# Optimization experiments

Measured on AMD Instinct MI355X. Metric: run time of the kernel, lower is better.

Reference implementation:

```python
import jax, jax.numpy as jnp
import numpy as np

N_HEADS = 8
NEG_INF = -1e9


def setup_inputs() -> dict:
    key = jax.random.key(0)
    ks = jax.random.split(key, 9)
    B, S, D = 4, 2048, 512
    scale = 1.0 / np.sqrt(D)
    x = jax.random.normal(ks[0], (B, S, D), dtype=jnp.float32)
    mask = jnp.tril(jnp.ones((S, S), dtype=bool))[None, None, :, :]  # causal [1,1,S,S]
    W_Q_w = jax.random.normal(ks[1], (D, D), dtype=jnp.float32) * scale
    W_Q_b = jax.random.normal(ks[2], (D,), dtype=jnp.float32) * 0.02
    W_K_w = jax.random.normal(ks[3], (D, D), dtype=jnp.float32) * scale
    W_K_b = jax.random.normal(ks[4], (D,), dtype=jnp.float32) * 0.02
    W_V_w = jax.random.normal(ks[5], (D, D), dtype=jnp.float32) * scale
    W_V_b = jax.random.normal(ks[6], (D,), dtype=jnp.float32) * 0.02
    W_O_w = jax.random.normal(ks[7], (D, D), dtype=jnp.float32) * scale
    W_O_b = jax.random.normal(ks[8], (D,), dtype=jnp.float32) * 0.02
    return {"x": x, "mask": mask,
            "W_Q_w": W_Q_w, "W_Q_b": W_Q_b, "W_K_w": W_K_w, "W_K_b": W_K_b,
            "W_V_w": W_V_w, "W_V_b": W_V_b, "W_O_w": W_O_w, "W_O_b": W_O_b}


def reference(x, mask, W_Q_w, W_Q_b, W_K_w, W_K_b, W_V_w, W_V_b, W_O_w, W_O_b):
    B, S, D = x.shape
    H = N_HEADS
    Dh = D // H
    # projections (torch Linear: x @ W.T + b), split heads -> [B,H,S,Dh]
    def split_heads(t):
        return t.reshape(B, S, H, Dh).transpose(0, 2, 1, 3)
    Q = split_heads(x @ W_Q_w.T + W_Q_b)
    K = split_heads(x @ W_K_w.T + W_K_b)
    V = split_heads(x @ W_V_w.T + W_V_b)
    # scaled dot-product attention with explicit [B,H,S,S] scores
    scores = jnp.einsum("bhqd,bhkd->bhqk", Q, K) / jnp.sqrt(jnp.float32(Dh))
    scores = jnp.where(mask, scores, jnp.float32(NEG_INF))
    att = jax.nn.softmax(scores, axis=-1)
    out = jnp.einsum("bhqk,bhkd->bhqd", att, V)
    out = out.transpose(0, 2, 1, 3).reshape(B, S, D)
    return out @ W_O_w.T + W_O_b
```

## Files before the change

kernel.cpp:

```cpp
#include <hip/hip_runtime.h>
#include <hip/hip_bf16.h>

#define BATCH 4
#define SEQ   2048
#define DIM   512
#define NH    8
#define DH    64
#define NTOK  (BATCH*SEQ)

typedef __bf16 bf16x8 __attribute__((ext_vector_type(8)));
typedef float  f32x4  __attribute__((ext_vector_type(4)));

#define MFMA16(a,b,c) __builtin_amdgcn_mfma_f32_16x16x32_bf16((a),(b),(c),0,0,0)

__global__ __launch_bounds__(256) void cvt_f32_bf16(const float* __restrict__ src,
                                                    __bf16* __restrict__ dst, int n8) {
  int i = blockIdx.x * blockDim.x + threadIdx.x;
  if (i >= n8) return;
  const float4* s = (const float4*)src;
  float4 a = s[2*i], b = s[2*i+1];
  bf16x8 o;
  o[0] = (__bf16)a.x; o[1] = (__bf16)a.y; o[2] = (__bf16)a.z; o[3] = (__bf16)a.w;
  o[4] = (__bf16)b.x; o[5] = (__bf16)b.y; o[6] = (__bf16)b.z; o[7] = (__bf16)b.w;
  *(bf16x8*)&dst[8*i] = o;
}

__global__ __launch_bounds__(256) void cvt_weights(
    const float* __restrict__ s0, const float* __restrict__ s1,
    const float* __restrict__ s2, const float* __restrict__ s3,
    __bf16* __restrict__ o0, __bf16* __restrict__ o1,
    __bf16* __restrict__ o2, __bf16* __restrict__ o3) {
  int i = blockIdx.x * blockDim.x + threadIdx.x;
  const int which = i >> 15, off = i & 32767;
  const float* src = (which == 0) ? s0 : (which == 1) ? s1 : (which == 2) ? s2 : s3;
  __bf16* dst      = (which == 0) ? o0 : (which == 1) ? o1 : (which == 2) ? o2 : o3;
  const float4* s = (const float4*)src;
  float4 a = s[2*off], b = s[2*off+1];
  bf16x8 o;
  o[0] = (__bf16)a.x; o[1] = (__bf16)a.y; o[2] = (__bf16)a.z; o[3] = (__bf16)a.w;
  o[4] = (__bf16)b.x; o[5] = (__bf16)b.y; o[6] = (__bf16)b.z; o[7] = (__bf16)b.w;
  *(bf16x8*)&dst[8*off] = o;
}

__global__ __launch_bounds__(256) void gemm_qkv(
    const __bf16* __restrict__ xb,
    const __bf16* __restrict__ wq, const __bf16* __restrict__ wk,
    const __bf16* __restrict__ wv,
    const float* __restrict__ bq, const float* __restrict__ bk,
    const float* __restrict__ bv,
    __bf16* __restrict__ Qb, __bf16* __restrict__ Kb, __bf16* __restrict__ Vt)
{
  const int z = blockIdx.z;
  const __bf16* W    = (z == 0) ? wq : (z == 1) ? wk : wv;
  const float*  bias = (z == 0) ? bq : (z == 1) ? bk : bv;

  __shared__ __bf16 As[128*72];
  __shared__ __bf16 Bs[128*72];

  const int tid  = threadIdx.x;
  const int m0   = blockIdx.x * 128, n0 = blockIdx.y * 128;
  const int w    = tid >> 6, lane = tid & 63, quad = lane >> 4, l16 = lane & 15;
  const int wm   = (w >> 1) * 64, wn = (w & 1) * 64;

  f32x4 acc[4][4] = {};

  for (int k0 = 0; k0 < DIM; k0 += 64) {
#pragma unroll
    for (int i = 0; i < 4; ++i) {
      int c   = tid + i * 256;
      int row = c >> 3;
      int kc  = (c & 7) << 3;
      *(bf16x8*)&As[row*72 + kc] = *(const bf16x8*)&xb[(size_t)(m0+row)*DIM + k0 + kc];
      *(bf16x8*)&Bs[row*72 + kc] = *(const bf16x8*)&W [(size_t)(n0+row)*DIM + k0 + kc];
    }
    __syncthreads();
#pragma unroll
    for (int kk = 0; kk < 2; ++kk) {
      const int ko = kk*32 + quad*8;
      bf16x8 af[4], bfr[4];
#pragma unroll
      for (int f = 0; f < 4; ++f) {
        af[f]  = *(const bf16x8*)&As[(wm + f*16 + l16)*72 + ko];
        bfr[f] = *(const bf16x8*)&Bs[(wn + f*16 + l16)*72 + ko];
      }
#pragma unroll
      for (int fm = 0; fm < 4; ++fm)
#pragma unroll
        for (int fn = 0; fn < 4; ++fn)
          acc[fm][fn] = MFMA16(af[fm], bfr[fn], acc[fm][fn]);
    }
    __syncthreads();
  }

#pragma unroll
  for (int fm = 0; fm < 4; ++fm) {
#pragma unroll
    for (int fn = 0; fn < 4; ++fn) {
      const int col  = n0 + wn + fn*16 + l16;
      const float bc = bias[col];
      const int h = col >> 6, dh = col & 63;
#pragma unroll
      for (int r = 0; r < 4; ++r) {
        const int row = m0 + wm + fm*16 + quad*4 + r;
        const int b = row >> 11, s = row & 2047;
        const float v = acc[fm][fn][r] + bc;
        if (z == 2) {
          Vt[((size_t)(b*NH + h)*DH + dh)*SEQ + s] = (__bf16)v;
        } else {
          __bf16* O = (z == 0) ? Qb : Kb;
          O[((size_t)(b*NH + h)*SEQ + s)*DH + dh] = (__bf16)v;
        }
      }
    }
  }
}

__global__ __launch_bounds__(256) void gemm_out(
    const __bf16* __restrict__ attnb, const __bf16* __restrict__ wo,
    const float* __restrict__ bo, float* __restrict__ out)
{
  __shared__ __bf16 As[128*72];
  __shared__ __bf16 Bs[128*72];

  const int tid = threadIdx.x;
  const int m0  = blockIdx.x * 128, n0 = blockIdx.y * 128;
  const int w   = tid >> 6, lane = tid & 63, quad = lane >> 4, l16 = lane & 15;
  const int wm  = (w >> 1) * 64, wn = (w & 1) * 64;

  f32x4 acc[4][4] = {};

  for (int k0 = 0; k0 < DIM; k0 += 64) {
#pragma unroll
    for (int i = 0; i < 4; ++i) {
      int c   = tid + i * 256;
      int row = c >> 3;
      int kc  = (c & 7) << 3;
      *(bf16x8*)&As[row*72 + kc] = *(const bf16x8*)&attnb[(size_t)(m0+row)*DIM + k0 + kc];
      *(bf16x8*)&Bs[row*72 + kc] = *(const bf16x8*)&wo   [(size_t)(n0+row)*DIM + k0 + kc];
    }
    __syncthreads();
#pragma unroll
    for (int kk = 0; kk < 2; ++kk) {
      const int ko = kk*32 + quad*8;
      bf16x8 af[4], bfr[4];
#pragma unroll
      for (int f = 0; f < 4; ++f) {
        af[f]  = *(const bf16x8*)&As[(wm + f*16 + l16)*72 + ko];
        bfr[f] = *(const bf16x8*)&Bs[(wn + f*16 + l16)*72 + ko];
      }
#pragma unroll
      for (int fm = 0; fm < 4; ++fm)
#pragma unroll
        for (int fn = 0; fn < 4; ++fn)
          acc[fm][fn] = MFMA16(af[fm], bfr[fn], acc[fm][fn]);
    }
    __syncthreads();
  }

#pragma unroll
  for (int fm = 0; fm < 4; ++fm) {
#pragma unroll
    for (int fn = 0; fn < 4; ++fn) {
      const int col  = n0 + wn + fn*16 + l16;
      const float bc = bo[col];
#pragma unroll
      for (int r = 0; r < 4; ++r) {
        const int row = m0 + wm + fm*16 + quad*4 + r;
        out[(size_t)row*DIM + col] = acc[fm][fn][r] + bc;
      }
    }
  }
}

__global__ __launch_bounds__(64) void flash_attn(
    const __bf16* __restrict__ Qb, const __bf16* __restrict__ Kb,
    const __bf16* __restrict__ Vt, __bf16* __restrict__ attnb)
{
  const int idx = blockIdx.x;
  const int bh  = idx & 31;
  const int t   = 63 - (idx >> 5);
  const int b   = bh >> 3, h = bh & 7;
  const int lane = threadIdx.x & 63, quad = lane >> 4, l16 = lane & 15;
  const int q0  = t * 32;

  const __bf16* Qp = Qb + (size_t)bh * SEQ * DH;
  const __bf16* Kp = Kb + (size_t)bh * SEQ * DH;
  const __bf16* Vp = Vt + (size_t)bh * DH * SEQ;

  __shared__ __bf16 Pw[32*72];

  bf16x8 qf[2][2];
#pragma unroll
  for (int mf = 0; mf < 2; ++mf)
#pragma unroll
    for (int kk = 0; kk < 2; ++kk) {
      bf16x8 q = *(const bf16x8*)&Qp[(size_t)(q0 + mf*16 + l16)*DH + kk*32 + quad*8];
#pragma unroll
      for (int j = 0; j < 8; ++j) q[j] = (__bf16)((float)q[j] * 0.125f);
      qf[mf][kk] = q;
    }

  f32x4 of[2][4] = {};
  float m_[2][4], l_[2][4];
#pragma unroll
  for (int mf = 0; mf < 2; ++mf)
#pragma unroll
    for (int r = 0; r < 4; ++r) { m_[mf][r] = -1e30f; l_[mf][r] = 0.f; }

  const int ktiles = (q0 >> 6) + 1;

  bf16x8 kfA[4][2], kfB[4][2];
#pragma unroll
  for (int fn = 0; fn < 4; ++fn)
#pragma unroll
    for (int kk = 0; kk < 2; ++kk)
      kfA[fn][kk] = *(const bf16x8*)&Kp[(size_t)(fn*16 + l16)*DH + kk*32 + quad*8];

#define TILE_STEP(KC, KN, KT)                                                  \
  {                                                                            \
    const int k0 = (KT) * 64;                                                  \
                   \
    bf16x8 vf[4][2];                                                           \
    _Pragma("unroll")                                                          \
    for (int nd = 0; nd < 4; ++nd)                                             \
      _Pragma("unroll")                                                        \
      for (int kq = 0; kq < 2; ++kq)                                           \
        vf[nd][kq] = *(const bf16x8*)&Vp[(size_t)(nd*16 + l16)*SEQ + k0 +      \
                                         kq*32 + quad*8];                      \
                               \
    {                                                                          \
      const int kn0 = ((KT) + 1 < ktiles) ? k0 + 64 : 0;                       \
      _Pragma("unroll")                                                        \
      for (int fn = 0; fn < 4; ++fn)                                           \
        _Pragma("unroll")                                                      \
        for (int kk = 0; kk < 2; ++kk)                                         \
          KN[fn][kk] = *(const bf16x8*)&Kp[(size_t)(kn0 + fn*16 + l16)*DH +    \
                                           kk*32 + quad*8];                    \
    }                                                                          \
                                            \
    f32x4 sf[2][4] = {};                                                       \
    _Pragma("unroll")                                                          \
    for (int mf = 0; mf < 2; ++mf)                                             \
      _Pragma("unroll")                                                        \
      for (int fn = 0; fn < 4; ++fn) {                                         \
        sf[mf][fn] = MFMA16(qf[mf][0], KC[fn][0], sf[mf][fn]);                 \
        sf[mf][fn] = MFMA16(qf[mf][1], KC[fn][1], sf[mf][fn]);                 \
      }                                                                        \
                            \
    if (k0 + 63 > q0) {                                                        \
      _Pragma("unroll")                                                        \
      for (int mf = 0; mf < 2; ++mf)                                           \
        _Pragma("unroll")                                                      \
        for (int fn = 0; fn < 4; ++fn) {                                       \
          const int col = k0 + fn*16 + l16;                                    \
          _Pragma("unroll")                                                    \
          for (int r = 0; r < 4; ++r) {                                        \
            const int row = q0 + mf*16 + quad*4 + r;                           \
            if (col > row) sf[mf][fn][r] = -1e30f;                             \
          }                                                                    \
        }                                                                      \
    }                                                                          \
                                        \
    float rmax[2][4];                                                          \
    _Pragma("unroll")                                                          \
    for (int mf = 0; mf < 2; ++mf)                                             \
      _Pragma("unroll")                                                        \
      for (int r = 0; r < 4; ++r)                                              \
        rmax[mf][r] = fmaxf(fmaxf(sf[mf][0][r], sf[mf][1][r]),                 \
                            fmaxf(sf[mf][2][r], sf[mf][3][r]));                \
    _Pragma("unroll")                                                          \
    for (int d = 1; d < 16; d <<= 1)                                           \
      _Pragma("unroll")                                                        \
      for (int mf = 0; mf < 2; ++mf)                                           \
        _Pragma("unroll")                                                      \
        for (int r = 0; r < 4; ++r)                                            \
          rmax[mf][r] = fmaxf(rmax[mf][r], __shfl_xor(rmax[mf][r], d));        \
    _Pragma("unroll")                                                          \
    for (int mf = 0; mf < 2; ++mf)                                             \
      _Pragma("unroll")                                                        \
      for (int r = 0; r < 4; ++r) {                                            \
        const float mn = fmaxf(m_[mf][r], rmax[mf][r]);                        \
        const float al = __expf(m_[mf][r] - mn);                               \
        m_[mf][r] = mn;                                                        \
        l_[mf][r] *= al;                                                       \
        _Pragma("unroll")                                                      \
        for (int nd = 0; nd < 4; ++nd) of[mf][nd][r] *= al;                    \
      }                                                                        \
    _Pragma("unroll")                                                          \
    for (int mf = 0; mf < 2; ++mf)                                             \
      _Pragma("unroll")                                                        \
      for (int fn = 0; fn < 4; ++fn)                                           \
        _Pragma("unroll")                                                      \
        for (int r = 0; r < 4; ++r)                                            \
          sf[mf][fn][r] = __expf(sf[mf][fn][r] - m_[mf][r]);                   \
    float rsum[2][4];                                                          \
    _Pragma("unroll")                                                          \
    for (int mf = 0; mf < 2; ++mf)                                             \
      _Pragma("unroll")                                                        \
      for (int r = 0; r < 4; ++r)                                              \
        rsum[mf][r] = (sf[mf][0][r] + sf[mf][1][r]) +                          \
                      (sf[mf][2][r] + sf[mf][3][r]);                           \
    _Pragma("unroll")                                                          \
    for (int d = 1; d < 16; d <<= 1)                                           \
      _Pragma("unroll")                                                        \
      for (int mf = 0; mf < 2; ++mf)                                           \
        _Pragma("unroll")                                                      \
        for (int r = 0; r < 4; ++r)                                            \
          rsum[mf][r] += __shfl_xor(rsum[mf][r], d);                           \
    _Pragma("unroll")                                                          \
    for (int mf = 0; mf < 2; ++mf)                                             \
      _Pragma("unroll")                                                        \
      for (int r = 0; r < 4; ++r) l_[mf][r] += rsum[mf][r];                    \
                                           \
    _Pragma("unroll")                                                          \
    for (int mf = 0; mf < 2; ++mf)                                             \
      _Pragma("unroll")                                                        \
      for (int fn = 0; fn < 4; ++fn)                                           \
        _Pragma("unroll")                                                      \
        for (int r = 0; r < 4; ++r)                                            \
          Pw[(mf*16 + quad*4 + r)*72 + fn*16 + l16] = (__bf16)sf[mf][fn][r];   \
    bf16x8 pa[2][2];                                                           \
    _Pragma("unroll")                                                          \
    for (int mf = 0; mf < 2; ++mf)                                             \
      _Pragma("unroll")                                                        \
      for (int kq = 0; kq < 2; ++kq)                                           \
        pa[mf][kq] = *(const bf16x8*)&Pw[(mf*16 + l16)*72 + kq*32 + quad*8];   \
                                                      \
    _Pragma("unroll")                                                          \
    for (int mf = 0; mf < 2; ++mf)                                             \
      _Pragma("unroll")                                                        \
      for (int nd = 0; nd < 4; ++nd) {                                         \
        of[mf][nd] = MFMA16(pa[mf][0], vf[nd][0], of[mf][nd]);                 \
        of[mf][nd] = MFMA16(pa[mf][1], vf[nd][1], of[mf][nd]);                 \
      }                                                                        \
  }

  for (int kt = 0; kt < ktiles; kt += 2) {
    TILE_STEP(kfA, kfB, kt);
    if (kt + 1 < ktiles) TILE_STEP(kfB, kfA, kt + 1);
  }
#undef TILE_STEP

#pragma unroll
  for (int mf = 0; mf < 2; ++mf)
#pragma unroll
    for (int r = 0; r < 4; ++r)
      l_[mf][r] = 1.0f / l_[mf][r];
#pragma unroll
  for (int mf = 0; mf < 2; ++mf)
#pragma unroll
    for (int nd = 0; nd < 4; ++nd) {
      const int dh = nd*16 + l16;
#pragma unroll
      for (int r = 0; r < 4; ++r) {
        const int q = q0 + mf*16 + quad*4 + r;
        attnb[((size_t)b*SEQ + q)*DIM + h*DH + dh] = (__bf16)(of[mf][nd][r] * l_[mf][r]);
      }
    }
}

extern "C" void kernel_launch(void* const* d_in, const int* in_sizes, int n_in,
                              void* d_out, int out_size, void* d_ws, size_t ws_size,
                              hipStream_t stream) {
  const float* x  = (const float*)d_in[0];
  const float* Wq = (const float*)d_in[2];
  const float* bq = (const float*)d_in[3];
  const float* Wk = (const float*)d_in[4];
  const float* bk = (const float*)d_in[5];
  const float* Wv = (const float*)d_in[6];
  const float* bv = (const float*)d_in[7];
  const float* Wo = (const float*)d_in[8];
  const float* bo = (const float*)d_in[9];
  float* out = (float*)d_out;

  __bf16* xb    = (__bf16*)d_ws;
  __bf16* wq    = xb + (size_t)NTOK*DIM;
  __bf16* wk    = wq + DIM*DIM;
  __bf16* wv    = wk + DIM*DIM;
  __bf16* wo    = wv + DIM*DIM;
  __bf16* Qb    = wo + DIM*DIM;
  __bf16* Kb    = Qb + (size_t)NTOK*DIM;
  __bf16* Vt    = Kb + (size_t)NTOK*DIM;
  __bf16* attnb = Vt + (size_t)NTOK*DIM;

  cvt_f32_bf16<<<(NTOK*DIM/8)/256, 256, 0, stream>>>(x, xb, NTOK*DIM/8);
  cvt_weights<<<(4*DIM*DIM/8)/256, 256, 0, stream>>>(Wq, Wk, Wv, Wo, wq, wk, wv, wo);

  gemm_qkv<<<dim3(NTOK/128, DIM/128, 3), 256, 0, stream>>>(
      xb, wq, wk, wv, bq, bk, bv, Qb, Kb, Vt);

  flash_attn<<<2048, 64, 0, stream>>>(Qb, Kb, Vt, attnb);

  gemm_out<<<dim3(NTOK/128, DIM/128), 256, 0, stream>>>(attnb, wo, bo, out);
}
```

Measured before the change: 211.3 us.

## Split attention KV loop across four waves and use async LDS loads in GEMMs

Flash attention now launches 256 threads per block. The KV tile range is split across four waves, and each wave keeps its own running max and sum; the partial outputs are merged through shared memory with a log-sum-exp rescale before a single vectorized store. The QKV and output GEMMs switch to global_load_lds direct-to-LDS copies with unpadded 64-wide rows. The QKV epilogue now stages results in an XOR-swizzled LDS tile so that Q, K and the transposed V are written with coalesced 16-byte stores. Together these aim to raise occupancy and parallelism on long causal rows and to remove scattered 2-byte global writes. The cost is an extra reduction with serialized syncs in attention, and the unpadded LDS reads in the GEMMs risk bank conflicts.

```diff
diff --git a/kernel.cpp b/kernel.cpp
--- a/kernel.cpp
+++ b/kernel.cpp
@@ -12,6 +12,12 @@
 typedef float  f32x4  __attribute__((ext_vector_type(4)));
 
 #define MFMA16(a,b,c) __builtin_amdgcn_mfma_f32_16x16x32_bf16((a),(b),(c),0,0,0)
+
+__device__ __forceinline__ void async_ld16(const __bf16* g, __bf16* l) {
+  __builtin_amdgcn_global_load_lds(
+      (const __attribute__((address_space(1))) void*)g,
+      (__attribute__((address_space(3))) void*)l, 16, 0, 0);
+}
 
 __global__ __launch_bounds__(256) void cvt_f32_bf16(const float* __restrict__ src,
                                                     __bf16* __restrict__ dst, int n8) {
@@ -54,24 +60,28 @@
   const __bf16* W    = (z == 0) ? wq : (z == 1) ? wk : wv;
   const float*  bias = (z == 0) ? bq : (z == 1) ? bk : bv;
 
-  __shared__ __bf16 As[128*72];
-  __shared__ __bf16 Bs[128*72];
+  __shared__ __bf16 S[2][128*64];
+  __bf16* As = S[0];
+  __bf16* Bs = S[1];
 
   const int tid  = threadIdx.x;
   const int m0   = blockIdx.x * 128, n0 = blockIdx.y * 128;
   const int w    = tid >> 6, lane = tid & 63, quad = lane >> 4, l16 = lane & 15;
   const int wm   = (w >> 1) * 64, wn = (w & 1) * 64;
+  const int lrow = lane >> 3;
+  const int lcol = (lane & 7) * 8;
 
   f32x4 acc[4][4] = {};
 
+  const __bf16* Ag = xb + (size_t)m0 * DIM;
+  const __bf16* Bg = W  + (size_t)n0 * DIM;
+
   for (int k0 = 0; k0 < DIM; k0 += 64) {
 #pragma unroll
     for (int i = 0; i < 4; ++i) {
-      int c   = tid + i * 256;
-      int row = c >> 3;
-      int kc  = (c & 7) << 3;
-      *(bf16x8*)&As[row*72 + kc] = *(const bf16x8*)&xb[(size_t)(m0+row)*DIM + k0 + kc];
-      *(bf16x8*)&Bs[row*72 + kc] = *(const bf16x8*)&W [(size_t)(n0+row)*DIM + k0 + kc];
+      const int rb = w*32 + i*8;
+      async_ld16(&Ag[(size_t)(rb + lrow)*DIM + k0 + lcol], &As[rb*64]);
+      async_ld16(&Bg[(size_t)(rb + lrow)*DIM + k0 + lcol], &Bs[rb*64]);
     }
     __syncthreads();
 #pragma unroll
@@ -80,8 +90,8 @@
       bf16x8 af[4], bfr[4];
 #pragma unroll
       for (int f = 0; f < 4; ++f) {
-        af[f]  = *(const bf16x8*)&As[(wm + f*16 + l16)*72 + ko];
-        bfr[f] = *(const bf16x8*)&Bs[(wn + f*16 + l16)*72 + ko];
+        af[f]  = *(const bf16x8*)&As[(wm + f*16 + l16)*64 + ko];
+        bfr[f] = *(const bf16x8*)&Bs[(wn + f*16 + l16)*64 + ko];
       }
 #pragma unroll
       for (int fm = 0; fm < 4; ++fm)
@@ -92,24 +102,59 @@
     __syncthreads();
   }
 
-#pragma unroll
-  for (int fm = 0; fm < 4; ++fm) {
-#pragma unroll
-    for (int fn = 0; fn < 4; ++fn) {
-      const int col  = n0 + wn + fn*16 + l16;
-      const float bc = bias[col];
-      const int h = col >> 6, dh = col & 63;
-#pragma unroll
-      for (int r = 0; r < 4; ++r) {
-        const int row = m0 + wm + fm*16 + quad*4 + r;
-        const int b = row >> 11, s = row & 2047;
-        const float v = acc[fm][fn][r] + bc;
-        if (z == 2) {
-          Vt[((size_t)(b*NH + h)*DH + dh)*SEQ + s] = (__bf16)v;
-        } else {
-          __bf16* O = (z == 0) ? Qb : Kb;
-          O[((size_t)(b*NH + h)*SEQ + s)*DH + dh] = (__bf16)v;
+  __bf16* Cs = &S[0][0];
+  if (z < 2) {
+#pragma unroll
+    for (int fm = 0; fm < 4; ++fm)
+#pragma unroll
+      for (int fn = 0; fn < 4; ++fn) {
+        const int col = wn + fn*16 + l16;
+        const float bc = bias[n0 + col];
+        const int chunk = col >> 3, ce = col & 7;
+#pragma unroll
+        for (int r = 0; r < 4; ++r) {
+          const int row = wm + fm*16 + quad*4 + r;
+          Cs[row*128 + ((chunk ^ (row & 7)) << 3) + ce] = (__bf16)(acc[fm][fn][r] + bc);
         }
+      }
+  } else {
+#pragma unroll
+    for (int fm = 0; fm < 4; ++fm)
+#pragma unroll
+      for (int fn = 0; fn < 4; ++fn) {
+        const int dhcol = wn + fn*16 + l16;
+        const float bc = bias[n0 + dhcol];
+        const int sbase = wm + fm*16 + quad*4;
+        const int schunk = sbase >> 3, so = sbase & 7;
+        __bf16* p = &Cs[dhcol*128 + ((schunk ^ (dhcol & 7)) << 3) + so];
+#pragma unroll
+        for (int r = 0; r < 4; ++r)
+          p[r] = (__bf16)(acc[fm][fn][r] + bc);
+      }
+  }
+  __syncthreads();
+  {
+    const int row = tid >> 1, half = tid & 1;
+    if (z < 2) {
+      __bf16* O = (z == 0) ? Qb : Kb;
+      const int s = m0 + row, bb = s >> 11, ss = s & 2047;
+#pragma unroll
+      for (int j = 0; j < 8; ++j) {
+        const int chunk = half*8 + j;
+        bf16x8 v = *(const bf16x8*)&Cs[row*128 + ((chunk ^ (row & 7)) << 3)];
+        const int colg = n0 + chunk*8;
+        const int hh = colg >> 6, dh = colg & 63;
+        *(bf16x8*)&O[((size_t)(bb*NH + hh)*SEQ + ss)*DH + dh] = v;
+      }
+    } else {
+      const int colg = n0 + row;
+      const int hh = colg >> 6, dh = colg & 63;
+      const int bb = m0 >> 11, s0s = m0 & 2047;
+#pragma unroll
+      for (int j = 0; j < 8; ++j) {
+        const int chunk = half*8 + j;
+        bf16x8 v = *(const bf16x8*)&Cs[row*128 + ((chunk ^ (row & 7)) << 3)];
+        *(bf16x8*)&Vt[((size_t)(bb*NH + hh)*DH + dh)*SEQ + s0s + chunk*8] = v;
       }
     }
   }
@@ -119,24 +164,27 @@
     const __bf16* __restrict__ attnb, const __bf16* __restrict__ wo,
     const float* __restrict__ bo, float* __restrict__ out)
 {
-  __shared__ __bf16 As[128*72];
-  __shared__ __bf16 Bs[128*72];
+  __shared__ __bf16 S[2][128*64];
+  __bf16* As = S[0];
+  __bf16* Bs = S[1];
 
   const int tid = threadIdx.x;
   const int m0  = blockIdx.x * 128, n0 = blockIdx.y * 128;
   const int w   = tid >> 6, lane = tid & 63, quad = lane >> 4, l16 = lane & 15;
   const int wm  = (w >> 1) * 64, wn = (w & 1) * 64;
+  const int lrow = lane >> 3, lcol = (lane & 7) * 8;
 
   f32x4 acc[4][4] = {};
 
+  const __bf16* Ag = attnb + (size_t)m0 * DIM;
+  const __bf16* Bg = wo    + (size_t)n0 * DIM;
+
   for (int k0 = 0; k0 < DIM; k0 += 64) {
 #pragma unroll
     for (int i = 0; i < 4; ++i) {
-      int c   = tid + i * 256;
-      int row = c >> 3;
-      int kc  = (c & 7) << 3;
-      *(bf16x8*)&As[row*72 + kc] = *(const bf16x8*)&attnb[(size_t)(m0+row)*DIM + k0 + kc];
-      *(bf16x8*)&Bs[row*72 + kc] = *(const bf16x8*)&wo   [(size_t)(n0+row)*DIM + k0 + kc];
+      const int rb = w*32 + i*8;
+      async_ld16(&Ag[(size_t)(rb + lrow)*DIM + k0 + lcol], &As[rb*64]);
+      async_ld16(&Bg[(size_t)(rb + lrow)*DIM + k0 + lcol], &Bs[rb*64]);
     }
     __syncthreads();
 #pragma unroll
@@ -145,8 +193,8 @@
       bf16x8 af[4], bfr[4];
 #pragma unroll
       for (int f = 0; f < 4; ++f) {
-        af[f]  = *(const bf16x8*)&As[(wm + f*16 + l16)*72 + ko];
-        bfr[f] = *(const bf16x8*)&Bs[(wn + f*16 + l16)*72 + ko];
+        af[f]  = *(const bf16x8*)&As[(wm + f*16 + l16)*64 + ko];
+        bfr[f] = *(const bf16x8*)&Bs[(wn + f*16 + l16)*64 + ko];
       }
 #pragma unroll
       for (int fm = 0; fm < 4; ++fm)
@@ -172,22 +220,26 @@
   }
 }
 
-__global__ __launch_bounds__(64) void flash_attn(
+__global__ __launch_bounds__(256) void flash_attn(
     const __bf16* __restrict__ Qb, const __bf16* __restrict__ Kb,
     const __bf16* __restrict__ Vt, __bf16* __restrict__ attnb)
 {
   const int idx = blockIdx.x;
   const int bh  = idx & 31;
-  const int t   = 63 - (idx >> 5);
+  const int qt  = 63 - (idx >> 5);
   const int b   = bh >> 3, h = bh & 7;
-  const int lane = threadIdx.x & 63, quad = lane >> 4, l16 = lane & 15;
-  const int q0  = t * 32;
+  const int tid = threadIdx.x;
+  const int w   = tid >> 6, lane = tid & 63, quad = lane >> 4, l16 = lane & 15;
+  const int q0  = qt * 32;
 
   const __bf16* Qp = Qb + (size_t)bh * SEQ * DH;
   const __bf16* Kp = Kb + (size_t)bh * SEQ * DH;
   const __bf16* Vp = Vt + (size_t)bh * DH * SEQ;
 
-  __shared__ __bf16 Pw[32*72];
+  __shared__ __bf16 Plds[4][32*72];
+  __shared__ float  OaccL[32*68];
+  __shared__ float  mL[4][32], lL[4][32];
+  __bf16* Pw = Plds[w];
 
   bf16x8 qf[2][2];
 #pragma unroll
@@ -207,19 +259,22 @@
 #pragma unroll
     for (int r = 0; r < 4; ++r) { m_[mf][r] = -1e30f; l_[mf][r] = 0.f; }
 
-  const int ktiles = (q0 >> 6) + 1;
-
-  bf16x8 kfA[4][2], kfB[4][2];
-#pragma unroll
-  for (int fn = 0; fn < 4; ++fn)
-#pragma unroll
-    for (int kk = 0; kk < 2; ++kk)
-      kfA[fn][kk] = *(const bf16x8*)&Kp[(size_t)(fn*16 + l16)*DH + kk*32 + quad*8];
+  const int nt  = (q0 >> 6) + 1;
+  const int c   = (nt + 3) >> 2;
+  const int ktb = w * c;
+  const int kte = (ktb + c < nt) ? (ktb + c) : nt;
+
+  if (ktb < kte) {
+    bf16x8 kfA[4][2], kfB[4][2];
+#pragma unroll
+    for (int fn = 0; fn < 4; ++fn)
+#pragma unroll
+      for (int kk = 0; kk < 2; ++kk)
+        kfA[fn][kk] = *(const bf16x8*)&Kp[(size_t)(ktb*64 + fn*16 + l16)*DH + kk*32 + quad*8];
 
 #define TILE_STEP(KC, KN, KT)                                                  \
   {                                                                            \
     const int k0 = (KT) * 64;                                                  \
-                   \
     bf16x8 vf[4][2];                                                           \
     _Pragma("unroll")                                                          \
     for (int nd = 0; nd < 4; ++nd)                                             \
@@ -227,9 +282,8 @@
       for (int kq = 0; kq < 2; ++kq)                                           \
         vf[nd][kq] = *(const bf16x8*)&Vp[(size_t)(nd*16 + l16)*SEQ + k0 +      \
                                          kq*32 + quad*8];                      \
-                               \
     {                                                                          \
-      const int kn0 = ((KT) + 1 < ktiles) ? k0 + 64 : 0;                       \
+      const int kn0 = ((KT) + 1 < kte) ? k0 + 64 : k0;                         \
       _Pragma("unroll")                                                        \
       for (int fn = 0; fn < 4; ++fn)                                           \
         _Pragma("unroll")                                                      \
@@ -237,7 +291,6 @@
           KN[fn][kk] = *(const bf16x8*)&Kp[(size_t)(kn0 + fn*16 + l16)*DH +    \
                                            kk*32 + quad*8];                    \
     }                                                                          \
-                                            \
     f32x4 sf[2][4] = {};                                                       \
     _Pragma("unroll")                                                          \
     for (int mf = 0; mf < 2; ++mf)                                             \
@@ -246,7 +299,6 @@
         sf[mf][fn] = MFMA16(qf[mf][0], KC[fn][0], sf[mf][fn]);                 \
         sf[mf][fn] = MFMA16(qf[mf][1], KC[fn][1], sf[mf][fn]);                 \
       }                                                                        \
-                            \
     if (k0 + 63 > q0) {                                                        \
       _Pragma("unroll")                                                        \
       for (int mf = 0; mf < 2; ++mf)                                           \
@@ -260,7 +312,6 @@
           }                                                                    \
         }                                                                      \
     }                                                                          \
-                                        \
     float rmax[2][4];                                                          \
     _Pragma("unroll")                                                          \
     for (int mf = 0; mf < 2; ++mf)                                             \
@@ -311,7 +362,6 @@
     for (int mf = 0; mf < 2; ++mf)                                             \
       _Pragma("unroll")                                                        \
       for (int r = 0; r < 4; ++r) l_[mf][r] += rsum[mf][r];                    \
-                                           \
     _Pragma("unroll")                                                          \
     for (int mf = 0; mf < 2; ++mf)                                             \
       _Pragma("unroll")                                                        \
@@ -325,7 +375,6 @@
       _Pragma("unroll")                                                        \
       for (int kq = 0; kq < 2; ++kq)                                           \
         pa[mf][kq] = *(const bf16x8*)&Pw[(mf*16 + l16)*72 + kq*32 + quad*8];   \
-                                                      \
     _Pragma("unroll")                                                          \
     for (int mf = 0; mf < 2; ++mf)                                             \
       _Pragma("unroll")                                                        \
@@ -335,28 +384,66 @@
       }                                                                        \
   }
 
-  for (int kt = 0; kt < ktiles; kt += 2) {
-    TILE_STEP(kfA, kfB, kt);
-    if (kt + 1 < ktiles) TILE_STEP(kfB, kfA, kt + 1);
-  }
+    for (int kt = ktb; kt < kte; kt += 2) {
+      TILE_STEP(kfA, kfB, kt);
+      if (kt + 1 < kte) TILE_STEP(kfB, kfA, kt + 1);
+    }
 #undef TILE_STEP
+  }
 
 #pragma unroll
   for (int mf = 0; mf < 2; ++mf)
 #pragma unroll
-    for (int r = 0; r < 4; ++r)
-      l_[mf][r] = 1.0f / l_[mf][r];
+    for (int r = 0; r < 4; ++r) {
+      const int row = mf*16 + quad*4 + r;
+      mL[w][row] = m_[mf][r];
+      lL[w][row] = l_[mf][r];
+    }
+  __syncthreads();
+
 #pragma unroll
   for (int mf = 0; mf < 2; ++mf)
 #pragma unroll
-    for (int nd = 0; nd < 4; ++nd) {
-      const int dh = nd*16 + l16;
-#pragma unroll
-      for (int r = 0; r < 4; ++r) {
-        const int q = q0 + mf*16 + quad*4 + r;
-        attnb[((size_t)b*SEQ + q)*DIM + h*DH + dh] = (__bf16)(of[mf][nd][r] * l_[mf][r]);
-      }
-    }
+    for (int r = 0; r < 4; ++r) {
+      const int row = mf*16 + quad*4 + r;
+      const float M = fmaxf(fmaxf(mL[0][row], mL[1][row]),
+                            fmaxf(mL[2][row], mL[3][row]));
+      const float al = __expf(m_[mf][r] - M);
+#pragma unroll
+      for (int nd = 0; nd < 4; ++nd) of[mf][nd][r] *= al;
+    }
+
+  for (int ww = 0; ww < 4; ++ww) {
+    if (w == ww) {
+#pragma unroll
+      for (int mf = 0; mf < 2; ++mf)
+#pragma unroll
+        for (int nd = 0; nd < 4; ++nd)
+#pragma unroll
+          for (int r = 0; r < 4; ++r) {
+            const int a = (mf*16 + quad*4 + r)*68 + nd*16 + l16;
+            if (ww == 0) OaccL[a] = of[mf][nd][r];
+            else         OaccL[a] += of[mf][nd][r];
+          }
+    }
+    __syncthreads();
+  }
+
+  {
+    const int row = tid >> 3, d0 = (tid & 7) * 8;
+    const float M = fmaxf(fmaxf(mL[0][row], mL[1][row]),
+                          fmaxf(mL[2][row], mL[3][row]));
+    float lt = 0.f;
+#pragma unroll
+    for (int ww = 0; ww < 4; ++ww)
+      lt += __expf(mL[ww][row] - M) * lL[ww][row];
+    const float inv = 1.0f / lt;
+    bf16x8 o;
+#pragma unroll
+    for (int j = 0; j < 8; ++j)
+      o[j] = (__bf16)(OaccL[row*68 + d0 + j] * inv);
+    *(bf16x8*)&attnb[((size_t)b*SEQ + q0 + row)*DIM + h*DH + d0] = o;
+  }
 }
 
 extern "C" void kernel_launch(void* const* d_in, const int* in_sizes, int n_in,
@@ -389,7 +476,7 @@
   gemm_qkv<<<dim3(NTOK/128, DIM/128, 3), 256, 0, stream>>>(
       xb, wq, wk, wv, bq, bk, bv, Qb, Kb, Vt);
 
-  flash_attn<<<2048, 64, 0, stream>>>(Qb, Kb, Vt, attnb);
+  flash_attn<<<2048, 256, 0, stream>>>(Qb, Kb, Vt, attnb);
 
   gemm_out<<<dim3(NTOK/128, DIM/128), 256, 0, stream>>>(attnb, wo, bo, out);
 }
```

After: 248.7 us. +17.7%, slower.
